# Kernel tuning notes

Hardware: AMD Instinct MI355X
Metric: run time of the kernel (lower is better)

Reference implementation:

```python
import jax, jax.numpy as jnp
import numpy as np

B, D_IN, H, D_OUT = 1024, 512, 512, 512


def _act(v):
    # torch.relu(x) ** 2
    r = jnp.maximum(v, 0.0)
    return r * r


def setup_inputs() -> dict:
    key = jax.random.key(0)
    ks = jax.random.split(key, 8)
    x = jax.random.normal(ks[0], (B, D_IN), dtype=jnp.float32)
    # input_to_hidden: Linear(D_IN, H)
    W_in = jax.random.normal(ks[1], (D_IN, H), dtype=jnp.float32) / np.sqrt(D_IN)
    b_in = jax.random.normal(ks[2], (H,), dtype=jnp.float32) * 0.01
    # hidden_to_hidden[i]: Linear(1, H-i-1). Pack into padded arrays [H-1, H]
    # where row i, column j is the weight feeding output index j (valid only j > i).
    W_hh = jax.random.normal(ks[3], (H - 1, H), dtype=jnp.float32) * 0.02
    b_hh = jax.random.normal(ks[4], (H - 1, H), dtype=jnp.float32) * 0.01
    # hidden_to_output: Linear(H, D_OUT)
    W_out = jax.random.normal(ks[5], (H, D_OUT), dtype=jnp.float32) / np.sqrt(H)
    b_out = jax.random.normal(ks[6], (D_OUT,), dtype=jnp.float32) * 0.01
    return {"x": x, "W_in": W_in, "b_in": b_in, "W_hh": W_hh, "b_hh": b_hh,
            "W_out": W_out, "b_out": b_out}


def reference(x, W_in, b_in, W_hh, b_hh, W_out, b_out):
    h0 = _act(x @ W_in + b_in)  # [B, H]
    hid = h0.shape[1]
    col = jnp.arange(hid)

    def step(h, inp):
        i, w, b = inp  # w, b: [H] padded rows
        src = jnp.take(h, i, axis=1)  # [B], uses UPDATED h (strict sequential dep)
        contrib = _act(src[:, None] * w[None, :] + b[None, :])  # [B, H]
        mask = (col > i).astype(h.dtype)  # only columns i+1.. get updated
        return h + contrib * mask[None, :], None

    xs = (jnp.arange(hid - 1), W_hh, b_hh)
    h, _ = jax.lax.scan(step, h0, xs)
    return h @ W_out + b_out  # [B, D_OUT]
```

## Files before the change

kernel.cpp:

```cpp
#include <hip/hip_runtime.h>
#include <hip/hip_fp16.h>

#define B_SZ 1024
#define DIN 512
#define HH 512
#define DOUT 512

typedef unsigned int uint32;

__device__ __forceinline__ float rl(float x, int i) {
    return __uint_as_float(__builtin_amdgcn_readlane(__float_as_uint(x), i));
}

__global__ __launch_bounds__(256)
void prep_kernel(const float* __restrict__ W_hh,
                 const float* __restrict__ b_hh,
                 uint32* __restrict__ wb) {
    int idx = blockIdx.x * 256 + threadIdx.x;
    int i = idx >> 9;
    int j = idx & 511;
    float w, b;
    if (j > i) { w = W_hh[idx]; b = b_hh[idx]; }
    else       { w = 0.0f;      b = -1.0f;     }
    __half2 p = __floats2half2_rn(w, b);
    wb[idx] = *(const uint32*)&p;
}

template <bool ACT>
__global__ __launch_bounds__(256)
void gemm_kernel(const float* __restrict__ A,
                 const float* __restrict__ Bm,
                 const float* __restrict__ bias,
                 float* __restrict__ C,
                 int M, int N, int K) {
    __shared__ float As[32][65];
    __shared__ float Bs[32][33];

    const int tid = threadIdx.x;
    const int bm = blockIdx.x * 64;
    const int bn = blockIdx.y * 32;
    const int ty = tid >> 4;
    const int tx = tid & 15;
    const int am = tid >> 2;
    const int ak = (tid & 3) * 8;
    const int bk = tid >> 3;
    const int bc = (tid & 7) * 4;

    float4 a0, a1, b0;
    auto stage = [&](int kt) {
        a0 = *(const float4*)&A[(size_t)(bm + am) * K + kt + ak];
        a1 = *(const float4*)&A[(size_t)(bm + am) * K + kt + ak + 4];
        b0 = *(const float4*)&Bm[(size_t)(kt + bk) * N + bn + bc];
    };

    float acc[4][2] = {};

    stage(0);
    for (int kt = 0; kt < K; kt += 32) {
        __syncthreads();
        #pragma unroll
        for (int u = 0; u < 4; ++u) {
            As[ak + u][am]     = ((const float*)&a0)[u];
            As[ak + 4 + u][am] = ((const float*)&a1)[u];
        }
        *(float4*)&Bs[bk][bc] = b0;
        __syncthreads();
        if (kt + 32 < K) stage(kt + 32);
        __builtin_amdgcn_sched_barrier(0);

        #pragma unroll
        for (int k = 0; k < 32; ++k) {
            const float4 a = *(const float4*)&As[k][4 * ty];
            const float2 b = *(const float2*)&Bs[k][2 * tx];
            acc[0][0] = fmaf(a.x, b.x, acc[0][0]);
            acc[0][1] = fmaf(a.x, b.y, acc[0][1]);
            acc[1][0] = fmaf(a.y, b.x, acc[1][0]);
            acc[1][1] = fmaf(a.y, b.y, acc[1][1]);
            acc[2][0] = fmaf(a.z, b.x, acc[2][0]);
            acc[2][1] = fmaf(a.z, b.y, acc[2][1]);
            acc[3][0] = fmaf(a.w, b.x, acc[3][0]);
            acc[3][1] = fmaf(a.w, b.y, acc[3][1]);
        }
    }

    const int col = bn + 2 * tx;
    const float2 bias2 = *(const float2*)&bias[col];
    #pragma unroll
    for (int j = 0; j < 4; ++j) {
        float2 v;
        v.x = acc[j][0] + bias2.x;
        v.y = acc[j][1] + bias2.y;
        if (ACT) {
            v.x = fmaxf(v.x, 0.f); v.x *= v.x;
            v.y = fmaxf(v.y, 0.f); v.y *= v.y;
        }
        *(float2*)&C[(size_t)(bm + 4 * ty + j) * N + col] = v;
    }
}

template <int C>
__device__ __forceinline__ void phase_fn(const uint32* __restrict__ wb,
                                         uint32* __restrict__ band,
                                         float* __restrict__ hpub,
                                         float& hr0, float& hr1,
                                         float& hr2, float& hr3,
                                         int lane, int wv, int tid) {
    constexpr int WC = 512 - 64 * C;
    constexpr int W4 = WC / 4;
    constexpr int NQ = (64 * W4) / 512;

    {
        const uint32* srow = wb + (size_t)(64 * C) * 512 + 64 * C;
        #pragma unroll
        for (int q = 0; q < NQ; ++q) {
            const int e4 = tid + 512 * q;
            const int r  = e4 / W4;
            const int c4 = e4 - r * W4;
            const uint4 v = *(const uint4*)&srow[(size_t)r * 512 + 4 * c4];
            *(uint4*)&band[r * WC + 4 * c4] = v;
        }
    }
    __syncthreads();

    if (wv == C) {
        uint32 ring[8];
        #pragma unroll
        for (int u = 0; u < 8; ++u) ring[u] = band[u * WC + lane];
        #pragma unroll 1
        for (int i8 = 0; i8 < 8; ++i8) {
            #pragma unroll
            for (int u = 0; u < 8; ++u) {
                const int i = 8 * i8 + u;
                const float2 w = __half22float2(*(const __half2*)&ring[u]);
                if (i8 < 7) ring[u] = band[(i + 8) * WC + lane];
                float t;
                t = fmaf(rl(hr0, i), w.x, w.y); t = fmaxf(t, 0.f); hr0 = fmaf(t, t, hr0);
                t = fmaf(rl(hr1, i), w.x, w.y); t = fmaxf(t, 0.f); hr1 = fmaf(t, t, hr1);
                t = fmaf(rl(hr2, i), w.x, w.y); t = fmaxf(t, 0.f); hr2 = fmaf(t, t, hr2);
                t = fmaf(rl(hr3, i), w.x, w.y); t = fmaxf(t, 0.f); hr3 = fmaf(t, t, hr3);
            }
        }
        hpub[0 * 64 + lane] = hr0;
        hpub[1 * 64 + lane] = hr1;
        hpub[2 * 64 + lane] = hr2;
        hpub[3 * 64 + lane] = hr3;
    }
    __syncthreads();

    if (wv > C) {
        const int cb = 64 * (wv - C);
        const float h0 = hpub[0 * 64 + lane];
        const float h1 = hpub[1 * 64 + lane];
        const float h2 = hpub[2 * 64 + lane];
        const float h3 = hpub[3 * 64 + lane];
        #pragma unroll 1
        for (int i8 = 0; i8 < 8; ++i8) {
            uint32 wr8[8];
            #pragma unroll
            for (int u = 0; u < 8; ++u)
                wr8[u] = band[(8 * i8 + u) * WC + cb + lane];
            #pragma unroll
            for (int u = 0; u < 8; ++u) {
                const int i = 8 * i8 + u;
                const float2 w = __half22float2(*(const __half2*)&wr8[u]);
                float t;
                t = fmaf(rl(h0, i), w.x, w.y); t = fmaxf(t, 0.f); hr0 = fmaf(t, t, hr0);
                t = fmaf(rl(h1, i), w.x, w.y); t = fmaxf(t, 0.f); hr1 = fmaf(t, t, hr1);
                t = fmaf(rl(h2, i), w.x, w.y); t = fmaxf(t, 0.f); hr2 = fmaf(t, t, hr2);
                t = fmaf(rl(h3, i), w.x, w.y); t = fmaxf(t, 0.f); hr3 = fmaf(t, t, hr3);
            }
        }
    }
    __syncthreads();
}

__global__ __launch_bounds__(512)
void scan_kernel(const uint32* __restrict__ wb, float* __restrict__ h) {
    __shared__ uint32 band[64 * 512];
    __shared__ float  hpub[4 * 64];

    const int tid  = threadIdx.x;
    const int lane = tid & 63;
    const int wv   = tid >> 6;
    const int r0   = blockIdx.x * 4;

    const size_t hb = (size_t)r0 * HH + 64 * wv + lane;
    float hr0 = h[hb];
    float hr1 = h[hb + HH];
    float hr2 = h[hb + 2 * HH];
    float hr3 = h[hb + 3 * HH];

    phase_fn<0>(wb, band, hpub, hr0, hr1, hr2, hr3, lane, wv, tid);
    phase_fn<1>(wb, band, hpub, hr0, hr1, hr2, hr3, lane, wv, tid);
    phase_fn<2>(wb, band, hpub, hr0, hr1, hr2, hr3, lane, wv, tid);
    phase_fn<3>(wb, band, hpub, hr0, hr1, hr2, hr3, lane, wv, tid);
    phase_fn<4>(wb, band, hpub, hr0, hr1, hr2, hr3, lane, wv, tid);
    phase_fn<5>(wb, band, hpub, hr0, hr1, hr2, hr3, lane, wv, tid);
    phase_fn<6>(wb, band, hpub, hr0, hr1, hr2, hr3, lane, wv, tid);
    phase_fn<7>(wb, band, hpub, hr0, hr1, hr2, hr3, lane, wv, tid);

    h[hb]          = hr0;
    h[hb + HH]     = hr1;
    h[hb + 2 * HH] = hr2;
    h[hb + 3 * HH] = hr3;
}

extern "C" void kernel_launch(void* const* d_in, const int* in_sizes, int n_in,
                              void* d_out, int out_size, void* d_ws, size_t ws_size,
                              hipStream_t stream) {
    const float* x     = (const float*)d_in[0];
    const float* W_in  = (const float*)d_in[1];
    const float* b_in  = (const float*)d_in[2];
    const float* W_hh  = (const float*)d_in[3];
    const float* b_hh  = (const float*)d_in[4];
    const float* W_out = (const float*)d_in[5];
    const float* b_out = (const float*)d_in[6];
    float* out = (float*)d_out;

    uint32* wb = (uint32*)d_ws;
    float*  h  = (float*)((char*)d_ws + (1u << 20));

    prep_kernel<<<dim3(1024), dim3(256), 0, stream>>>(W_hh, b_hh, wb);

    gemm_kernel<true><<<dim3(B_SZ / 64, HH / 32), dim3(256), 0, stream>>>(
        x, W_in, b_in, h, B_SZ, HH, DIN);

    scan_kernel<<<dim3(256), dim3(512), 0, stream>>>(wb, h);

    gemm_kernel<false><<<dim3(B_SZ / 64, DOUT / 32), dim3(256), 0, stream>>>(
        h, W_out, b_out, out, B_SZ, DOUT, HH);
}
```

Measured before the change: 183.4 us.

## Split scan weight band into halves and overlap loads with compute

The scan kernel splits each 64-row weight band into two 32-row halves in shared memory. Idle waves load the next half, or the next phase's first half, while the diagonal wave and the trailing waves compute, so global-to-LDS copies are hidden behind the sequential recurrence instead of stalling all waves at each phase start. The GEMM kernel is also double-buffered in LDS, which removes one barrier per k-tile. The cost is more barriers per phase, more complex indexing, and doubled GEMM shared memory, which may lower occupancy.

```diff
diff --git a/kernel.cpp b/kernel.cpp
--- a/kernel.cpp
+++ b/kernel.cpp
@@ -33,8 +33,8 @@
                  const float* __restrict__ bias,
                  float* __restrict__ C,
                  int M, int N, int K) {
-    __shared__ float As[32][65];
-    __shared__ float Bs[32][33];
+    __shared__ float As[2][32][65];
+    __shared__ float Bs[2][32][33];
 
     const int tid = threadIdx.x;
     const int bm = blockIdx.x * 64;
@@ -52,26 +52,28 @@
         a1 = *(const float4*)&A[(size_t)(bm + am) * K + kt + ak + 4];
         b0 = *(const float4*)&Bm[(size_t)(kt + bk) * N + bn + bc];
     };
+    auto commit = [&](int buf) {
+        #pragma unroll
+        for (int u = 0; u < 4; ++u) {
+            As[buf][ak + u][am]     = ((const float*)&a0)[u];
+            As[buf][ak + 4 + u][am] = ((const float*)&a1)[u];
+        }
+        *(float4*)&Bs[buf][bk][bc] = b0;
+    };
 
     float acc[4][2] = {};
 
     stage(0);
+    commit(0);
+    int cur = 0;
     for (int kt = 0; kt < K; kt += 32) {
         __syncthreads();
-        #pragma unroll
-        for (int u = 0; u < 4; ++u) {
-            As[ak + u][am]     = ((const float*)&a0)[u];
-            As[ak + 4 + u][am] = ((const float*)&a1)[u];
-        }
-        *(float4*)&Bs[bk][bc] = b0;
-        __syncthreads();
         if (kt + 32 < K) stage(kt + 32);
-        __builtin_amdgcn_sched_barrier(0);
 
         #pragma unroll
         for (int k = 0; k < 32; ++k) {
-            const float4 a = *(const float4*)&As[k][4 * ty];
-            const float2 b = *(const float2*)&Bs[k][2 * tx];
+            const float4 a = *(const float4*)&As[cur][k][4 * ty];
+            const float2 b = *(const float2*)&Bs[cur][k][2 * tx];
             acc[0][0] = fmaf(a.x, b.x, acc[0][0]);
             acc[0][1] = fmaf(a.x, b.y, acc[0][1]);
             acc[1][0] = fmaf(a.y, b.x, acc[1][0]);
@@ -81,6 +83,8 @@
             acc[3][0] = fmaf(a.w, b.x, acc[3][0]);
             acc[3][1] = fmaf(a.w, b.y, acc[3][1]);
         }
+        if (kt + 32 < K) commit(cur ^ 1);
+        cur ^= 1;
     }
 
     const int col = bn + 2 * tx;
@@ -100,39 +104,29 @@
 
 template <int C>
 __device__ __forceinline__ void phase_fn(const uint32* __restrict__ wb,
-                                         uint32* __restrict__ band,
+                                         uint32* __restrict__ bandA,
+                                         uint32* __restrict__ bandB,
                                          float* __restrict__ hpub,
                                          float& hr0, float& hr1,
                                          float& hr2, float& hr3,
-                                         int lane, int wv, int tid) {
+                                         int lane, int wv) {
     constexpr int WC = 512 - 64 * C;
     constexpr int W4 = WC / 4;
-    constexpr int NQ = (64 * W4) / 512;
-
-    {
-        const uint32* srow = wb + (size_t)(64 * C) * 512 + 64 * C;
-        #pragma unroll
-        for (int q = 0; q < NQ; ++q) {
-            const int e4 = tid + 512 * q;
-            const int r  = e4 / W4;
-            const int c4 = e4 - r * W4;
-            const uint4 v = *(const uint4*)&srow[(size_t)r * 512 + 4 * c4];
-            *(uint4*)&band[r * WC + 4 * c4] = v;
-        }
-    }
+    const uint32* brow = wb + (size_t)(64 * C) * 512 + 64 * C;
+
     __syncthreads();
 
     if (wv == C) {
         uint32 ring[8];
         #pragma unroll
-        for (int u = 0; u < 8; ++u) ring[u] = band[u * WC + lane];
+        for (int u = 0; u < 8; ++u) ring[u] = bandA[u * WC + lane];
         #pragma unroll 1
-        for (int i8 = 0; i8 < 8; ++i8) {
+        for (int i8 = 0; i8 < 4; ++i8) {
             #pragma unroll
             for (int u = 0; u < 8; ++u) {
                 const int i = 8 * i8 + u;
                 const float2 w = __half22float2(*(const __half2*)&ring[u]);
-                if (i8 < 7) ring[u] = band[(i + 8) * WC + lane];
+                if (i8 < 3) ring[u] = bandA[(i + 8) * WC + lane];
                 float t;
                 t = fmaf(rl(hr0, i), w.x, w.y); t = fmaxf(t, 0.f); hr0 = fmaf(t, t, hr0);
                 t = fmaf(rl(hr1, i), w.x, w.y); t = fmaxf(t, 0.f); hr1 = fmaf(t, t, hr1);
@@ -144,21 +138,57 @@
         hpub[1 * 64 + lane] = hr1;
         hpub[2 * 64 + lane] = hr2;
         hpub[3 * 64 + lane] = hr3;
-    }
+    } else {
+        const int p = (wv < C) ? wv : wv - 1;
+        const int pid = p * 64 + lane;
+        constexpr int TOT = 32 * W4;
+        #pragma unroll 4
+        for (int e4 = pid; e4 < TOT; e4 += 448) {
+            const int r = e4 / W4;
+            const int c4 = e4 - r * W4;
+            *(uint4*)&bandB[r * WC + 4 * c4] =
+                *(const uint4*)&brow[(size_t)(32 + r) * 512 + 4 * c4];
+        }
+    }
+
     __syncthreads();
 
-    if (wv > C) {
+    if (wv == C) {
+        uint32 ring[8];
+        #pragma unroll
+        for (int u = 0; u < 8; ++u) ring[u] = bandB[u * WC + lane];
+        #pragma unroll 1
+        for (int i8 = 0; i8 < 4; ++i8) {
+            #pragma unroll
+            for (int u = 0; u < 8; ++u) {
+                const int i = 32 + 8 * i8 + u;
+                const float2 w = __half22float2(*(const __half2*)&ring[u]);
+                if (i8 < 3) ring[u] = bandB[(8 * i8 + u + 8) * WC + lane];
+                float t;
+                t = fmaf(rl(hr0, i), w.x, w.y); t = fmaxf(t, 0.f); hr0 = fmaf(t, t, hr0);
+                t = fmaf(rl(hr1, i), w.x, w.y); t = fmaxf(t, 0.f); hr1 = fmaf(t, t, hr1);
+                t = fmaf(rl(hr2, i), w.x, w.y); t = fmaxf(t, 0.f); hr2 = fmaf(t, t, hr2);
+                t = fmaf(rl(hr3, i), w.x, w.y); t = fmaxf(t, 0.f); hr3 = fmaf(t, t, hr3);
+            }
+        }
+        if (lane >= 32) {
+            hpub[0 * 64 + lane] = hr0;
+            hpub[1 * 64 + lane] = hr1;
+            hpub[2 * 64 + lane] = hr2;
+            hpub[3 * 64 + lane] = hr3;
+        }
+    } else if (wv > C) {
         const int cb = 64 * (wv - C);
         const float h0 = hpub[0 * 64 + lane];
         const float h1 = hpub[1 * 64 + lane];
         const float h2 = hpub[2 * 64 + lane];
         const float h3 = hpub[3 * 64 + lane];
         #pragma unroll 1
-        for (int i8 = 0; i8 < 8; ++i8) {
+        for (int i8 = 0; i8 < 4; ++i8) {
             uint32 wr8[8];
             #pragma unroll
             for (int u = 0; u < 8; ++u)
-                wr8[u] = band[(8 * i8 + u) * WC + cb + lane];
+                wr8[u] = bandA[(8 * i8 + u) * WC + cb + lane];
             #pragma unroll
             for (int u = 0; u < 8; ++u) {
                 const int i = 8 * i8 + u;
@@ -171,12 +201,52 @@
             }
         }
     }
+
     __syncthreads();
+
+    if (wv > C) {
+        const int cb = 64 * (wv - C);
+        const float h0 = hpub[0 * 64 + lane];
+        const float h1 = hpub[1 * 64 + lane];
+        const float h2 = hpub[2 * 64 + lane];
+        const float h3 = hpub[3 * 64 + lane];
+        #pragma unroll 1
+        for (int i8 = 0; i8 < 4; ++i8) {
+            uint32 wr8[8];
+            #pragma unroll
+            for (int u = 0; u < 8; ++u)
+                wr8[u] = bandB[(8 * i8 + u) * WC + cb + lane];
+            #pragma unroll
+            for (int u = 0; u < 8; ++u) {
+                const int i = 32 + 8 * i8 + u;
+                const float2 w = __half22float2(*(const __half2*)&wr8[u]);
+                float t;
+                t = fmaf(rl(h0, i), w.x, w.y); t = fmaxf(t, 0.f); hr0 = fmaf(t, t, hr0);
+                t = fmaf(rl(h1, i), w.x, w.y); t = fmaxf(t, 0.f); hr1 = fmaf(t, t, hr1);
+                t = fmaf(rl(h2, i), w.x, w.y); t = fmaxf(t, 0.f); hr2 = fmaf(t, t, hr2);
+                t = fmaf(rl(h3, i), w.x, w.y); t = fmaxf(t, 0.f); hr3 = fmaf(t, t, hr3);
+            }
+        }
+    } else if (C < 7) {
+        constexpr int WN = WC - 64;
+        constexpr int WN4 = WN / 4;
+        constexpr int TOTN = 32 * WN4;
+        const uint32* nrow = wb + (size_t)(64 * (C + 1)) * 512 + 64 * (C + 1);
+        const int pid = wv * 64 + lane;
+        #pragma unroll 2
+        for (int e4 = pid; e4 < TOTN; e4 += 64 * (C + 1)) {
+            const int r = e4 / WN4;
+            const int c4 = e4 - r * WN4;
+            *(uint4*)&bandA[r * WN + 4 * c4] =
+                *(const uint4*)&nrow[(size_t)r * 512 + 4 * c4];
+        }
+    }
 }
 
 __global__ __launch_bounds__(512)
 void scan_kernel(const uint32* __restrict__ wb, float* __restrict__ h) {
-    __shared__ uint32 band[64 * 512];
+    __shared__ uint32 bandA[32 * 512];
+    __shared__ uint32 bandB[32 * 512];
     __shared__ float  hpub[4 * 64];
 
     const int tid  = threadIdx.x;
@@ -190,14 +260,22 @@
     float hr2 = h[hb + 2 * HH];
     float hr3 = h[hb + 3 * HH];
 
-    phase_fn<0>(wb, band, hpub, hr0, hr1, hr2, hr3, lane, wv, tid);
-    phase_fn<1>(wb, band, hpub, hr0, hr1, hr2, hr3, lane, wv, tid);
-    phase_fn<2>(wb, band, hpub, hr0, hr1, hr2, hr3, lane, wv, tid);
-    phase_fn<3>(wb, band, hpub, hr0, hr1, hr2, hr3, lane, wv, tid);
-    phase_fn<4>(wb, band, hpub, hr0, hr1, hr2, hr3, lane, wv, tid);
-    phase_fn<5>(wb, band, hpub, hr0, hr1, hr2, hr3, lane, wv, tid);
-    phase_fn<6>(wb, band, hpub, hr0, hr1, hr2, hr3, lane, wv, tid);
-    phase_fn<7>(wb, band, hpub, hr0, hr1, hr2, hr3, lane, wv, tid);
+    #pragma unroll 4
+    for (int e4 = tid; e4 < 32 * 128; e4 += 512) {
+        const int r = e4 >> 7;
+        const int c4 = e4 & 127;
+        *(uint4*)&bandA[r * 512 + 4 * c4] =
+            *(const uint4*)&wb[(size_t)r * 512 + 4 * c4];
+    }
+
+    phase_fn<0>(wb, bandA, bandB, hpub, hr0, hr1, hr2, hr3, lane, wv);
+    phase_fn<1>(wb, bandA, bandB, hpub, hr0, hr1, hr2, hr3, lane, wv);
+    phase_fn<2>(wb, bandA, bandB, hpub, hr0, hr1, hr2, hr3, lane, wv);
+    phase_fn<3>(wb, bandA, bandB, hpub, hr0, hr1, hr2, hr3, lane, wv);
+    phase_fn<4>(wb, bandA, bandB, hpub, hr0, hr1, hr2, hr3, lane, wv);
+    phase_fn<5>(wb, bandA, bandB, hpub, hr0, hr1, hr2, hr3, lane, wv);
+    phase_fn<6>(wb, bandA, bandB, hpub, hr0, hr1, hr2, hr3, lane, wv);
+    phase_fn<7>(wb, bandA, bandB, hpub, hr0, hr1, hr2, hr3, lane, wv);
 
     h[hb]          = hr0;
     h[hb + HH]     = hr1;
```

Result: faster. 178.3 us (-2.8%).
